# Kernel tuning notes

Measured on AMD Instinct MI355X. Metric: run time of the kernel, lower is better.

## Reference

```python
import jax, jax.numpy as jnp
import numpy as np
from jax import lax

B, E, D, N, R, K = 4, 768, 1536, 16, 48, 4
H, W = 16, 16
L = H * W
NDIR = 4


def _perms():
    idx = np.arange(L)
    idx_v = np.arange(L).reshape(H, W).T.reshape(-1)  # column-major (vertical) scan order
    perms = [idx, idx[::-1].copy(), idx_v, idx_v[::-1].copy()]
    invs = [np.argsort(p) for p in perms]
    return [jnp.asarray(p) for p in perms], [jnp.asarray(p) for p in invs]

PERMS, INVS = _perms()


def setup_inputs() -> dict:
    key = jax.random.key(0)
    ks = jax.random.split(key, 10)
    hidden_states = jax.random.normal(ks[0], (B, L, E), jnp.float32)
    in_proj_w = jax.random.normal(ks[1], (2 * D, E), jnp.float32) * 0.02
    out_proj_w = jax.random.normal(ks[2], (E, D), jnp.float32) * 0.02
    conv_w = jax.random.normal(ks[3], (NDIR, D, K), jnp.float32) * 0.1
    conv_b = jax.random.normal(ks[4], (NDIR, D), jnp.float32) * 0.1
    xproj_w = jax.random.normal(ks[5], (NDIR, R + 2 * N, D), jnp.float32) * 0.02
    dt_init_std = R ** -0.5
    dtproj_w = jax.random.uniform(ks[6], (NDIR, D, R), jnp.float32, -dt_init_std, dt_init_std)
    dt = jnp.exp(jax.random.uniform(ks[7], (NDIR, D), jnp.float32)
                 * (np.log(0.1) - np.log(0.001)) + np.log(0.001))
    dt = jnp.clip(dt, 1e-4, None)
    dtproj_b = dt + jnp.log(-jnp.expm1(-dt))  # inverse-softplus init as in the module
    A_log = jnp.broadcast_to(
        jnp.log(jnp.arange(1, N + 1, dtype=jnp.float32))[None, None, :], (NDIR, D, N)).copy()
    D_param = jnp.ones((NDIR, D), jnp.float32)
    return dict(hidden_states=hidden_states, in_proj_w=in_proj_w, out_proj_w=out_proj_w,
                conv_w=conv_w, conv_b=conv_b, xproj_w=xproj_w, dtproj_w=dtproj_w,
                dtproj_b=dtproj_b, A_log=A_log, D_param=D_param)


def _mamba_dir(xz, cw, cb, xw, dtw, dtb, a_log, dpar):
    # xz: (B, 2D, L) in this direction's scan order
    x, z = xz[:, :D], xz[:, D:]
    # causal depthwise conv1d + SiLU (mamba_inner_fn conv path)
    x = lax.conv_general_dilated(x, cw[:, None, :], (1,), [(K - 1, 0)],
                                 feature_group_count=D,
                                 dimension_numbers=('NCH', 'OIH', 'NCH'))
    x = jax.nn.silu(x + cb[None, :, None])
    # x_proj -> dt, B, C
    x_dbl = jnp.einsum('bdl,kd->bkl', x, xw)
    dt, Bm, Cm = x_dbl[:, :R], x_dbl[:, R:R + N], x_dbl[:, R + N:]
    delta = jax.nn.softplus(jnp.einsum('brl,dr->bdl', dt, dtw) + dtb[None, :, None])
    A = -jnp.exp(a_log)                                  # (D, N)
    dA = jnp.exp(jnp.einsum('bdl,dn->lbdn', delta, A))   # (L, B, D, N)
    dBu = jnp.einsum('bdl,bnl,bdl->lbdn', delta, Bm, x)  # delta * B * u

    def step(h, inp):
        da, dbu = inp
        h = da * h + dbu
        return h, h

    h0 = jnp.zeros((x.shape[0], D, N), x.dtype)
    _, hs = lax.scan(step, h0, (dA, dBu))                # (L, B, D, N)
    y = jnp.einsum('lbdn,bnl->bdl', hs, Cm) + dpar[None, :, None] * x
    return y * jax.nn.silu(z)                            # gate, (B, D, L)


def reference(hidden_states, in_proj_w, out_proj_w, conv_w, conv_b,
              xproj_w, dtproj_w, dtproj_b, A_log, D_param):
    xz = jnp.einsum('ble,fe->bfl', hidden_states, in_proj_w)  # (B, 2D, L)
    out = jnp.zeros((hidden_states.shape[0], D, L), hidden_states.dtype)
    for i in range(NDIR):  # fixed small set of structurally distinct scan directions
        xz_i = xz[:, :, PERMS[i]]
        y = _mamba_dir(xz_i, conv_w[i], conv_b[i], xproj_w[i], dtproj_w[i],
                       dtproj_b[i], A_log[i], D_param[i])
        out = out + y[:, :, INVS[i]]  # multi_reverse then sum-fusion
    return jnp.einsum('bdl,ed->ble', out, out_proj_w)
```

## Files before the change

### kernel.cpp

```cpp
#include <hip/hip_runtime.h>
#include <hip/hip_bf16.h>

#define BI   4
#define LI   256
#define EI   768
#define DI   1536
#define NI   16
#define RI   48
#define KI   4
#define NDIRS 4
#define F2D  3072
#define MROWS 1024
#define LOG2E 1.4426950408889634f

typedef float    floatx2 __attribute__((ext_vector_type(2)));
typedef float    floatx4 __attribute__((ext_vector_type(4)));
typedef _Float16 halfx2  __attribute__((ext_vector_type(2)));
typedef _Float16 halfx4  __attribute__((ext_vector_type(4)));
typedef _Float16 halfx8  __attribute__((ext_vector_type(8)));

typedef __attribute__((address_space(3))) unsigned lds_u32;
typedef __attribute__((address_space(1))) const unsigned glb_u32;

__device__ __forceinline__ void load16(const _Float16* g, _Float16* l) {
    __builtin_amdgcn_global_load_lds((glb_u32*)g, (lds_u32*)l, 16, 0, 0);
}

__device__ __forceinline__ int perm_idx(int dir, int j) {
    switch (dir) {
        case 0:  return j;
        case 1:  return 255 - j;
        case 2:  return ((j & 15) << 4) | (j >> 4);
        default: return 255 - (((j & 15) << 4) | (j >> 4));
    }
}

template<int CTRL>
__device__ __forceinline__ float dpp_add(float p) {
    int t = __builtin_amdgcn_update_dpp(0, __builtin_bit_cast(int, p),
                                        CTRL, 0xf, 0xf, true);
    return p + __builtin_bit_cast(float, t);
}
__device__ __forceinline__ float grp8_sum(float p) {
    p = dpp_add<0xB1>(p);
    p = dpp_add<0x4E>(p);
    p = dpp_add<0x141>(p);
    return p;
}

template<int BM, int BN, int WGN, int FM, int FN>
__device__ __forceinline__ void gemm_core(const _Float16* __restrict__ Ah,
                                          const _Float16* __restrict__ Al, int lda,
                                          const _Float16* __restrict__ Bh,
                                          const _Float16* __restrict__ Bl, int ldb,
                                          int nChunks, _Float16* smem,
                                          floatx4 (&acc)[FM][FN]) {
    const int tid = threadIdx.x, lane = tid & 63, wave = tid >> 6;
    const int wave_m = wave / WGN, wave_n = wave % WGN;
    _Float16* sAh = smem;
    _Float16* sAl = smem + BM * 32;
    _Float16* sBh = smem + BM * 64;
    _Float16* sBl = smem + BM * 64 + BN * 32;
    const int rr = lane & 15, koff = (lane >> 4) * 8;
    const int arow = wave_m * FM * 16, brow = wave_n * FN * 16;

    for (int c = 0; c < nChunks; ++c) {
        for (int idx = tid; idx < BM * 4; idx += 256) {
            int r = idx >> 2, s = (idx & 3) * 8;
            load16(Ah + (size_t)r * lda + c * 32 + s, sAh + idx * 8);
            load16(Al + (size_t)r * lda + c * 32 + s, sAl + idx * 8);
        }
        for (int idx = tid; idx < BN * 4; idx += 256) {
            int r = idx >> 2, s = (idx & 3) * 8;
            load16(Bh + (size_t)r * ldb + c * 32 + s, sBh + idx * 8);
            load16(Bl + (size_t)r * ldb + c * 32 + s, sBl + idx * 8);
        }
        asm volatile("s_waitcnt vmcnt(0)" ::: "memory");
        __syncthreads();

        halfx8 ahf[FM], alf[FM], bhf[FN], blf[FN];
        #pragma unroll
        for (int i = 0; i < FM; ++i) {
            ahf[i] = *(const halfx8*)(sAh + (arow + i * 16 + rr) * 32 + koff);
            alf[i] = *(const halfx8*)(sAl + (arow + i * 16 + rr) * 32 + koff);
        }
        #pragma unroll
        for (int j = 0; j < FN; ++j) {
            bhf[j] = *(const halfx8*)(sBh + (brow + j * 16 + rr) * 32 + koff);
            blf[j] = *(const halfx8*)(sBl + (brow + j * 16 + rr) * 32 + koff);
        }
        #pragma unroll
        for (int i = 0; i < FM; ++i)
            #pragma unroll
            for (int j = 0; j < FN; ++j) {
                acc[i][j] = __builtin_amdgcn_mfma_f32_16x16x32_f16(ahf[i], bhf[j], acc[i][j], 0, 0, 0);
                acc[i][j] = __builtin_amdgcn_mfma_f32_16x16x32_f16(ahf[i], blf[j], acc[i][j], 0, 0, 0);
                acc[i][j] = __builtin_amdgcn_mfma_f32_16x16x32_f16(alf[i], bhf[j], acc[i][j], 0, 0, 0);
            }
        __syncthreads();
    }
}

__global__ __launch_bounds__(256) void k_splitall(
        const float* __restrict__ hs,  const float* __restrict__ wip,
        const float* __restrict__ wop, const float* __restrict__ xw,
        const float* __restrict__ dtw,
        _Float16* __restrict__ hsh,  _Float16* __restrict__ hsl,
        _Float16* __restrict__ wiph, _Float16* __restrict__ wipl,
        _Float16* __restrict__ woph, _Float16* __restrict__ wopl,
        _Float16* __restrict__ xwh,  _Float16* __restrict__ xwl,
        _Float16* __restrict__ dtwh, _Float16* __restrict__ dtwl) {
    int i4 = (blockIdx.x * 256 + threadIdx.x) * 4;
    floatx4 v;
    _Float16 *dh, *dl; int off;
    if (i4 < 786432)        { off = i4;           v = *(const floatx4*)(hs + off);  dh = hsh;  dl = hsl;  }
    else if (i4 < 3145728)  { off = i4 - 786432;  v = *(const floatx4*)(wip + off); dh = wiph; dl = wipl; }
    else if (i4 < 4325376)  { off = i4 - 3145728; v = *(const floatx4*)(wop + off); dh = woph; dl = wopl; }
    else if (i4 < 4816896)  { off = i4 - 4325376; v = *(const floatx4*)(xw + off);  dh = xwh;  dl = xwl;  }
    else {
        int t0 = i4 - 4816896;
        int col = t0 & 63, dr = t0 >> 6;
        floatx4 z = {0.f, 0.f, 0.f, 0.f};
        v = (col < 48) ? *(const floatx4*)(dtw + (size_t)dr * 48 + col) : z;
        dh = dtwh; dl = dtwl; off = t0;
    }
    halfx4 hh, hl;
    #pragma unroll
    for (int e = 0; e < 4; ++e) {
        _Float16 h = (_Float16)v[e];
        hh[e] = h; hl[e] = (_Float16)(v[e] - (float)h);
    }
    *(halfx4*)(dh + off) = hh;
    *(halfx4*)(dl + off) = hl;
}

__global__ __launch_bounds__(256) void k_inproj_t(const _Float16* __restrict__ Ah,
                                                  const _Float16* __restrict__ Al,
                                                  const _Float16* __restrict__ Bh,
                                                  const _Float16* __restrict__ Bl,
                                                  float* __restrict__ C) {
    __shared__ _Float16 smem[128 * 64 + 128 * 64];
    int row0 = blockIdx.x * 128, col0 = blockIdx.y * 128, k0 = blockIdx.z * 384;
    float* Cp = C + (size_t)blockIdx.z * MROWS * F2D;
    floatx4 acc[4][4] = {};
    gemm_core<128, 128, 2, 4, 4>(Ah + (size_t)row0 * EI + k0, Al + (size_t)row0 * EI + k0, EI,
                                 Bh + (size_t)col0 * EI + k0, Bl + (size_t)col0 * EI + k0, EI,
                                 12, smem, acc);
    int lane = threadIdx.x & 63, wave = threadIdx.x >> 6;
    int cc = lane & 15, q = lane >> 4;
    int rbase = row0 + (wave >> 1) * 64, cbase = col0 + (wave & 1) * 64;
    #pragma unroll
    for (int i = 0; i < 4; ++i)
        #pragma unroll
        for (int j = 0; j < 4; ++j)
            #pragma unroll
            for (int r = 0; r < 4; ++r)
                Cp[(size_t)(rbase + i * 16 + q * 4 + r) * F2D + cbase + j * 16 + cc] = acc[i][j][r];
}

__global__ __launch_bounds__(256) void k_outproj_t(const _Float16* __restrict__ Ah,
                                                   const _Float16* __restrict__ Al,
                                                   const _Float16* __restrict__ Bh,
                                                   const _Float16* __restrict__ Bl,
                                                   float* __restrict__ C) {
    __shared__ _Float16 smem[192 * 64];
    int row0 = blockIdx.x * 64, col0 = blockIdx.y * 128, k0 = blockIdx.z * 384;
    float* Cp = C + (size_t)blockIdx.z * MROWS * EI;
    floatx4 acc[2][4] = {};
    gemm_core<64, 128, 2, 2, 4>(Ah + (size_t)row0 * DI + k0, Al + (size_t)row0 * DI + k0, DI,
                                Bh + (size_t)col0 * DI + k0, Bl + (size_t)col0 * DI + k0, DI,
                                12, smem, acc);
    int lane = threadIdx.x & 63, wave = threadIdx.x >> 6;
    int cc = lane & 15, q = lane >> 4;
    int rbase = row0 + (wave >> 1) * 32, cbase = col0 + (wave & 1) * 64;
    #pragma unroll
    for (int i = 0; i < 2; ++i)
        #pragma unroll
        for (int j = 0; j < 4; ++j)
            #pragma unroll
            for (int r = 0; r < 4; ++r)
                Cp[(size_t)(rbase + i * 16 + q * 4 + r) * EI + cbase + j * 16 + cc] = acc[i][j][r];
}

__global__ __launch_bounds__(256) void k_osum(const float* __restrict__ oacc,
                                              float* __restrict__ out) {
    int i4 = (blockIdx.x * 256 + threadIdx.x) * 4;
    const size_t S = (size_t)MROWS * EI;
    floatx4 s = *(const floatx4*)(oacc + i4) + *(const floatx4*)(oacc + S + i4) +
                *(const floatx4*)(oacc + 2 * S + i4) + *(const floatx4*)(oacc + 3 * S + i4);
    *(floatx4*)(out + i4) = s;
}

__global__ __launch_bounds__(256) void k_xdbl_t(const _Float16* __restrict__ xh,
                                                const _Float16* __restrict__ xl,
                                                const _Float16* __restrict__ xwh,
                                                const _Float16* __restrict__ xwl,
                                                float* __restrict__ C) {
    __shared__ _Float16 smem[208 * 64];
    int row0 = blockIdx.x * 128, dir = blockIdx.y, k0 = blockIdx.z * 192;
    float* Cp = C + (size_t)blockIdx.z * NDIRS * MROWS * 80;
    floatx4 acc[2][5] = {};
    const size_t abase = ((size_t)dir * MROWS + row0) * DI + k0;
    const size_t bbase = (size_t)dir * 80 * DI + k0;
    gemm_core<128, 80, 1, 2, 5>(xh + abase, xl + abase, DI,
                                xwh + bbase, xwl + bbase, DI, 6, smem, acc);
    int lane = threadIdx.x & 63, wave = threadIdx.x >> 6;
    int cc = lane & 15, q = lane >> 4;
    int rbase = row0 + wave * 32;
    #pragma unroll
    for (int i = 0; i < 2; ++i)
        #pragma unroll
        for (int j = 0; j < 5; ++j)
            #pragma unroll
            for (int r = 0; r < 4; ++r)
                Cp[((size_t)dir * MROWS + rbase + i * 16 + q * 4 + r) * 80 + j * 16 + cc] = acc[i][j][r];
}

__global__ __launch_bounds__(256) void k_xsplit(const float* __restrict__ acc,
                                                _Float16* __restrict__ dtqh,
                                                _Float16* __restrict__ dtql,
                                                float* __restrict__ BCm) {
    const size_t PS = (size_t)NDIRS * MROWS * 80;
    int idx = blockIdx.x * 256 + threadIdx.x;
    int dir = idx / (MROWS * 96);
    int rem = idx - dir * MROWS * 96;
    int row = rem / 96, col = rem - row * 96;
    size_t rbase = (size_t)dir * MROWS + row;
    auto sum8 = [&](int c) {
        size_t o = rbase * 80 + c;
        float s = 0.f;
        #pragma unroll
        for (int kp = 0; kp < 8; ++kp) s += acc[kp * PS + o];
        return s;
    };
    if (col < 64) {
        float v = (col < 48) ? sum8(col) : 0.f;
        _Float16 h = (_Float16)v;
        dtqh[rbase * 64 + col] = h;
        dtql[rbase * 64 + col] = (_Float16)(v - (float)h);
    } else if (col < 80) {
        int n = col - 64;
        BCm[rbase * 32 + n * 2] = sum8(48 + n);
    } else {
        int n = col - 80;
        BCm[rbase * 32 + n * 2 + 1] = sum8(64 + n);
    }
}

__global__ __launch_bounds__(256) void k_delta_t(const _Float16* __restrict__ dtqh,
                                                 const _Float16* __restrict__ dtql,
                                                 const _Float16* __restrict__ dtwh,
                                                 const _Float16* __restrict__ dtwl,
                                                 const float* __restrict__ dtb,
                                                 float* __restrict__ delta) {
    __shared__ _Float16 smem[192 * 64];
    int row0 = blockIdx.x * 64, col0 = blockIdx.y * 128, dir = blockIdx.z;
    floatx4 acc[2][4] = {};
    const size_t abase = ((size_t)dir * MROWS + row0) * 64;
    const size_t bbase = ((size_t)dir * DI + col0) * 64;
    gemm_core<64, 128, 2, 2, 4>(dtqh + abase, dtql + abase, 64,
                                dtwh + bbase, dtwl + bbase, 64, 2, smem, acc);
    int lane = threadIdx.x & 63, wave = threadIdx.x >> 6;
    int cc = lane & 15, q = lane >> 4;
    int rbase = row0 + (wave >> 1) * 32, cbase = col0 + (wave & 1) * 64;
    #pragma unroll
    for (int i = 0; i < 2; ++i)
        #pragma unroll
        for (int j = 0; j < 4; ++j) {
            int col = cbase + j * 16 + cc;
            float bias = dtb[(size_t)dir * DI + col];
            #pragma unroll
            for (int r = 0; r < 4; ++r) {
                float v = acc[i][j][r] + bias;
                float sp = (v > 20.f) ? v : log1pf(__expf(v));
                delta[((size_t)dir * MROWS + rbase + i * 16 + q * 4 + r) * DI + col] = sp;
            }
        }
}

__global__ __launch_bounds__(512) void k_conv4(const float* __restrict__ xz,
                                               const float* __restrict__ cw,
                                               const float* __restrict__ cb,
                                               _Float16* __restrict__ xh,
                                               _Float16* __restrict__ xl) {
    const size_t S = (size_t)MROWS * F2D;
    const int b = blockIdx.y, d0 = blockIdx.x * 16;
    const int tid = threadIdx.x;
    __shared__ float sx[256][18];

    for (int i = tid; i < 1024; i += 512) {
        int row = i >> 2, c4 = (i & 3) * 4;
        size_t o = ((size_t)b * 256 + row) * F2D + d0 + c4;
        floatx4 v = *(const floatx4*)(xz + o) + *(const floatx4*)(xz + S + o);
        floatx2 v0 = {v[0], v[1]}, v1 = {v[2], v[3]};
        *(floatx2*)&sx[row][c4]     = v0;
        *(floatx2*)&sx[row][c4 + 2] = v1;
    }
    __syncthreads();

    const int dsub = tid & 15, lg = tid >> 4;
    const int d = d0 + dsub, j0 = lg * 8;
    #pragma unroll
    for (int dir = 0; dir < NDIRS; ++dir) {
        floatx4 w = *(const floatx4*)(cw + ((size_t)dir * DI + d) * KI);
        float bias = cb[(size_t)dir * DI + d];
        float xm3 = (j0 >= 3) ? sx[perm_idx(dir, j0 - 3)][dsub] : 0.f;
        float xm2 = (j0 >= 2) ? sx[perm_idx(dir, j0 - 2)][dsub] : 0.f;
        float xm1 = (j0 >= 1) ? sx[perm_idx(dir, j0 - 1)][dsub] : 0.f;
        #pragma unroll
        for (int j = 0; j < 8; ++j) {
            float cur = sx[perm_idx(dir, j0 + j)][dsub];
            float s = bias + w[0] * xm3 + w[1] * xm2 + w[2] * xm1 + w[3] * cur;
            xm3 = xm2; xm2 = xm1; xm1 = cur;
            float x = s / (1.f + __expf(-s));
            _Float16 h = (_Float16)x;
            size_t o = ((size_t)dir * MROWS + b * 256 + j0 + j) * DI + d;
            xh[o] = h;
            xl[o] = (_Float16)(x - (float)h);
        }
    }
}

__global__ __launch_bounds__(256) void k_scan(const float* __restrict__ delta,
                                              const _Float16* __restrict__ xhg,
                                              const _Float16* __restrict__ xlg,
                                              const float* __restrict__ BCm,
                                              const float* __restrict__ A_log,
                                              const float* __restrict__ Dp,
                                              float* __restrict__ ydir) {
    const int dchunk = blockIdx.x, b = blockIdx.y, dir = blockIdx.z;
    const int tid = threadIdx.x;
    const int dslot = tid >> 3;
    const int np = tid & 7;
    const int d0 = dchunk * 32, d = d0 + dslot;

    __shared__ float sdx[2][32][68];
    __shared__ float sbc[2][32][32];
    __shared__ float sY[32][32];

    const float Av0 = -__expf(A_log[((size_t)dir * DI + d) * NI + 2 * np]) * LOG2E;
    const float Av1 = -__expf(A_log[((size_t)dir * DI + d) * NI + 2 * np + 1]) * LOG2E;
    const float Dpar = Dp[(size_t)dir * DI + d];
    float h0 = 0.f, h1 = 0.f;

    const size_t dirrow = (size_t)dir * MROWS;
    const int srow = tid >> 3, sc4 = (tid & 7) * 4;

    floatx4 rdel, rbc;
    halfx4 rxh, rxl;
    auto load_chunk = [&](int j0) {
        int row = b * 256 + j0 + srow;
        size_t o = (dirrow + row) * DI + d0 + sc4;
        rdel = *(const floatx4*)(delta + o);
        rxh  = *(const halfx4*)(xhg + o);
        rxl  = *(const halfx4*)(xlg + o);
        rbc  = *(const floatx4*)(BCm + (dirrow + row) * 32 + sc4);
    };

    load_chunk(0);

    for (int c = 0; c < 8; ++c) {
        const int buf = c & 1;
        #pragma unroll
        for (int e = 0; e < 4; ++e) {
            floatx2 t;
            t[0] = rdel[e];
            t[1] = (float)rxh[e] + (float)rxl[e];
            *(floatx2*)&sdx[buf][sc4 + e][srow * 2] = t;
        }
        *(floatx4*)&sbc[buf][srow][sc4] = rbc;
        __syncthreads();
        if (c < 7) load_chunk((c + 1) * 32);

        #pragma unroll
        for (int jj = 0; jj < 32; jj += 2) {
            floatx4 dxx = *(const floatx4*)&sdx[buf][dslot][jj * 2];
            #pragma unroll
            for (int t = 0; t < 2; ++t) {
                floatx4 bc = *(const floatx4*)&sbc[buf][jj + t][np * 4];
                float dv = dxx[t * 2], xv = dxx[t * 2 + 1];
                float a0 = __builtin_amdgcn_exp2f(dv * Av0);
                float a1 = __builtin_amdgcn_exp2f(dv * Av1);
                float du = dv * xv;
                h0 = fmaf(a0, h0, du * bc[0]);
                h1 = fmaf(a1, h1, du * bc[2]);
                float p = fmaf(h1, bc[3], h0 * bc[1]);
                p = grp8_sum(p);
                if (np == 0) sY[jj + t][dslot] = fmaf(Dpar, xv, p);
            }
        }
        __syncthreads();

        {
            int lout = perm_idx(dir, c * 32 + srow);
            floatx4 o = *(const floatx4*)&sY[srow][sc4];
            *(floatx4*)&ydir[(dirrow + (size_t)b * 256 + lout) * DI + d0 + sc4] = o;
        }
    }
}

__global__ __launch_bounds__(256) void k_sum(const float* __restrict__ ydir,
                                             const float* __restrict__ xz,
                                             _Float16* __restrict__ yh,
                                             _Float16* __restrict__ yl) {
    int i4 = (blockIdx.x * 256 + threadIdx.x) * 4;
    const size_t S = (size_t)MROWS * DI;
    const size_t SZ = (size_t)MROWS * F2D;
    int row = i4 / DI, dcol = i4 - row * DI;
    size_t zo = (size_t)row * F2D + DI + dcol;
    floatx4 zv = *(const floatx4*)(xz + zo) + *(const floatx4*)(xz + SZ + zo);
    floatx4 s = *(const floatx4*)(ydir + i4) + *(const floatx4*)(ydir + S + i4) +
                *(const floatx4*)(ydir + 2 * S + i4) + *(const floatx4*)(ydir + 3 * S + i4);
    halfx4 hh, hl;
    #pragma unroll
    for (int e = 0; e < 4; ++e) {
        float g = zv[e] / (1.f + __expf(-zv[e]));
        float v = s[e] * g;
        _Float16 h = (_Float16)v;
        hh[e] = h; hl[e] = (_Float16)(v - (float)h);
    }
    *(halfx4*)(yh + i4) = hh;
    *(halfx4*)(yl + i4) = hl;
}

extern "C" void kernel_launch(void* const* d_in, const int* in_sizes, int n_in,
                              void* d_out, int out_size, void* d_ws, size_t ws_size,
                              hipStream_t stream) {
    const float* hs   = (const float*)d_in[0];
    const float* wip  = (const float*)d_in[1];
    const float* wop  = (const float*)d_in[2];
    const float* cw   = (const float*)d_in[3];
    const float* cb   = (const float*)d_in[4];
    const float* xw   = (const float*)d_in[5];
    const float* dtw  = (const float*)d_in[6];
    const float* dtb  = (const float*)d_in[7];
    const float* alog = (const float*)d_in[8];
    const float* dpar = (const float*)d_in[9];
    float* out = (float*)d_out;

    char* p = (char*)d_ws;
    auto alloc_f32 = [&](size_t n) { float* r = (float*)p; p += n * 4; return r; };
    auto alloc_f16 = [&](size_t n) { _Float16* r = (_Float16*)p; p += n * 2; return r; };

    _Float16* hsh  = alloc_f16(786432);
    _Float16* hsl  = alloc_f16(786432);
    _Float16* wiph = alloc_f16(2359296);
    _Float16* wipl = alloc_f16(2359296);
    _Float16* woph = alloc_f16(1179648);
    _Float16* wopl = alloc_f16(1179648);
    _Float16* xwh  = alloc_f16(491520);
    _Float16* xwl  = alloc_f16(491520);
    _Float16* dtwh = alloc_f16((size_t)NDIRS * DI * 64);
    _Float16* dtwl = alloc_f16((size_t)NDIRS * DI * 64);
    float*    xz   = alloc_f32((size_t)2 * MROWS * F2D);
    _Float16* xh   = alloc_f16((size_t)NDIRS * MROWS * DI);
    _Float16* xl   = alloc_f16((size_t)NDIRS * MROWS * DI);
    _Float16* dtqh = alloc_f16((size_t)NDIRS * MROWS * 64);
    _Float16* dtql = alloc_f16((size_t)NDIRS * MROWS * 64);
    float*    BCm  = alloc_f32((size_t)NDIRS * MROWS * 32);
    float*    delta= alloc_f32((size_t)NDIRS * MROWS * DI);
    float*    ydir = alloc_f32((size_t)NDIRS * MROWS * DI);
    _Float16* yh   = alloc_f16((size_t)MROWS * DI);
    _Float16* yl   = alloc_f16((size_t)MROWS * DI);

    float* xdba = ydir;
    float* oacc = delta;

    k_splitall<<<dim3(5088), 256, 0, stream>>>(hs, wip, wop, xw, dtw,
                                               hsh, hsl, wiph, wipl, woph, wopl,
                                               xwh, xwl, dtwh, dtwl);
    k_inproj_t<<<dim3(8, 24, 2), 256, 0, stream>>>(hsh, hsl, wiph, wipl, xz);
    k_conv4   <<<dim3(96, BI), 512, 0, stream>>>(xz, cw, cb, xh, xl);
    k_xdbl_t  <<<dim3(8, NDIRS, 8), 256, 0, stream>>>(xh, xl, xwh, xwl, xdba);
    k_xsplit  <<<dim3(1536), 256, 0, stream>>>(xdba, dtqh, dtql, BCm);
    k_delta_t <<<dim3(16, 12, NDIRS), 256, 0, stream>>>(dtqh, dtql, dtwh, dtwl, dtb, delta);
    k_scan    <<<dim3(DI / 32, BI, NDIRS), 256, 0, stream>>>(delta, xh, xl, BCm,
                                                             alog, dpar, ydir);
    k_sum     <<<dim3(1536), 256, 0, stream>>>(ydir, xz, yh, yl);
    k_outproj_t<<<dim3(16, 6, 4), 256, 0, stream>>>(yh, yl, woph, wopl, oacc);
    k_osum    <<<dim3(768), 256, 0, stream>>>(oacc, out);
}
```

Baseline: 231.8 us.

## Fuse delta projection GEMM and softplus into the selective scan kernel

Removes the separate delta GEMM kernel. Inside the scan, each chunk of 32 timesteps now computes delta with split-fp16 MFMA (hi/lo products) from the dt-rank projections, applies the bias and softplus, and writes the result straight to shared memory. This avoids writing and re-reading the full fp32 delta tensor (4x1024x1536) through global memory and saves one launch. In exchange the scan loses its double-buffered LDS, adds a second barrier per chunk, and puts MFMA and log1p/exp work on the scan's critical path.

```diff
diff --git a/kernel.cpp b/kernel.cpp
--- a/kernel.cpp
+++ b/kernel.cpp
@@ -247,37 +247,6 @@
     }
 }
 
-__global__ __launch_bounds__(256) void k_delta_t(const _Float16* __restrict__ dtqh,
-                                                 const _Float16* __restrict__ dtql,
-                                                 const _Float16* __restrict__ dtwh,
-                                                 const _Float16* __restrict__ dtwl,
-                                                 const float* __restrict__ dtb,
-                                                 float* __restrict__ delta) {
-    __shared__ _Float16 smem[192 * 64];
-    int row0 = blockIdx.x * 64, col0 = blockIdx.y * 128, dir = blockIdx.z;
-    floatx4 acc[2][4] = {};
-    const size_t abase = ((size_t)dir * MROWS + row0) * 64;
-    const size_t bbase = ((size_t)dir * DI + col0) * 64;
-    gemm_core<64, 128, 2, 2, 4>(dtqh + abase, dtql + abase, 64,
-                                dtwh + bbase, dtwl + bbase, 64, 2, smem, acc);
-    int lane = threadIdx.x & 63, wave = threadIdx.x >> 6;
-    int cc = lane & 15, q = lane >> 4;
-    int rbase = row0 + (wave >> 1) * 32, cbase = col0 + (wave & 1) * 64;
-    #pragma unroll
-    for (int i = 0; i < 2; ++i)
-        #pragma unroll
-        for (int j = 0; j < 4; ++j) {
-            int col = cbase + j * 16 + cc;
-            float bias = dtb[(size_t)dir * DI + col];
-            #pragma unroll
-            for (int r = 0; r < 4; ++r) {
-                float v = acc[i][j][r] + bias;
-                float sp = (v > 20.f) ? v : log1pf(__expf(v));
-                delta[((size_t)dir * MROWS + rbase + i * 16 + q * 4 + r) * DI + col] = sp;
-            }
-        }
-}
-
 __global__ __launch_bounds__(512) void k_conv4(const float* __restrict__ xz,
                                                const float* __restrict__ cw,
                                                const float* __restrict__ cb,
@@ -321,7 +290,11 @@
     }
 }
 
-__global__ __launch_bounds__(256) void k_scan(const float* __restrict__ delta,
+__global__ __launch_bounds__(256) void k_scan(const _Float16* __restrict__ dtqh,
+                                              const _Float16* __restrict__ dtql,
+                                              const _Float16* __restrict__ dtwh,
+                                              const _Float16* __restrict__ dtwl,
+                                              const float* __restrict__ dtb,
                                               const _Float16* __restrict__ xhg,
                                               const _Float16* __restrict__ xlg,
                                               const float* __restrict__ BCm,
@@ -329,13 +302,13 @@
                                               const float* __restrict__ Dp,
                                               float* __restrict__ ydir) {
     const int dchunk = blockIdx.x, b = blockIdx.y, dir = blockIdx.z;
-    const int tid = threadIdx.x;
+    const int tid = threadIdx.x, lane = tid & 63, wave = tid >> 6;
     const int dslot = tid >> 3;
     const int np = tid & 7;
     const int d0 = dchunk * 32, d = d0 + dslot;
 
-    __shared__ float sdx[2][32][68];
-    __shared__ float sbc[2][32][32];
+    __shared__ float sdx[32][68];
+    __shared__ float sbc[32][32];
     __shared__ float sY[32][32];
 
     const float Av0 = -__expf(A_log[((size_t)dir * DI + d) * NI + 2 * np]) * LOG2E;
@@ -346,38 +319,68 @@
     const size_t dirrow = (size_t)dir * MROWS;
     const int srow = tid >> 3, sc4 = (tid & 7) * 4;
 
-    floatx4 rdel, rbc;
+    const int rowhalf = wave >> 1, dhalf = wave & 1;
+    const int rr = lane & 15, koff = (lane >> 4) * 8, q = lane >> 4;
+    const size_t bfb = ((size_t)dir * DI + d0 + dhalf * 16 + rr) * 64;
+    halfx8 bhf[2], blf[2];
+    bhf[0] = *(const halfx8*)(dtwh + bfb + koff);
+    bhf[1] = *(const halfx8*)(dtwh + bfb + 32 + koff);
+    blf[0] = *(const halfx8*)(dtwl + bfb + koff);
+    blf[1] = *(const halfx8*)(dtwl + bfb + 32 + koff);
+    const float bias = dtb[(size_t)dir * DI + d0 + dhalf * 16 + rr];
+
+    floatx4 rbc;
     halfx4 rxh, rxl;
     auto load_chunk = [&](int j0) {
         int row = b * 256 + j0 + srow;
         size_t o = (dirrow + row) * DI + d0 + sc4;
-        rdel = *(const floatx4*)(delta + o);
-        rxh  = *(const halfx4*)(xhg + o);
-        rxl  = *(const halfx4*)(xlg + o);
-        rbc  = *(const floatx4*)(BCm + (dirrow + row) * 32 + sc4);
+        rxh = *(const halfx4*)(xhg + o);
+        rxl = *(const halfx4*)(xlg + o);
+        rbc = *(const floatx4*)(BCm + (dirrow + row) * 32 + sc4);
     };
+    halfx8 ahf[2], alf[2];
+    auto load_afrag = [&](int c) {
+        size_t o = (dirrow + b * 256 + c * 32 + rowhalf * 16 + rr) * 64;
+        ahf[0] = *(const halfx8*)(dtqh + o + koff);
+        ahf[1] = *(const halfx8*)(dtqh + o + 32 + koff);
+        alf[0] = *(const halfx8*)(dtql + o + koff);
+        alf[1] = *(const halfx8*)(dtql + o + 32 + koff);
+    };
 
     load_chunk(0);
+    load_afrag(0);
 
     for (int c = 0; c < 8; ++c) {
-        const int buf = c & 1;
-        #pragma unroll
-        for (int e = 0; e < 4; ++e) {
-            floatx2 t;
-            t[0] = rdel[e];
-            t[1] = (float)rxh[e] + (float)rxl[e];
-            *(floatx2*)&sdx[buf][sc4 + e][srow * 2] = t;
-        }
-        *(floatx4*)&sbc[buf][srow][sc4] = rbc;
+        #pragma unroll
+        for (int e = 0; e < 4; ++e)
+            sdx[sc4 + e][srow * 2 + 1] = (float)rxh[e] + (float)rxl[e];
+        *(floatx4*)&sbc[srow][sc4] = rbc;
         __syncthreads();
-        if (c < 7) load_chunk((c + 1) * 32);
+
+        {
+            floatx4 acc = {};
+            #pragma unroll
+            for (int kc = 0; kc < 2; ++kc) {
+                acc = __builtin_amdgcn_mfma_f32_16x16x32_f16(ahf[kc], bhf[kc], acc, 0, 0, 0);
+                acc = __builtin_amdgcn_mfma_f32_16x16x32_f16(ahf[kc], blf[kc], acc, 0, 0, 0);
+                acc = __builtin_amdgcn_mfma_f32_16x16x32_f16(alf[kc], bhf[kc], acc, 0, 0, 0);
+            }
+            #pragma unroll
+            for (int r = 0; r < 4; ++r) {
+                float v = acc[r] + bias;
+                float sp = (v > 20.f) ? v : log1pf(__expf(v));
+                sdx[dhalf * 16 + rr][(rowhalf * 16 + q * 4 + r) * 2] = sp;
+            }
+        }
+        if (c < 7) { load_chunk((c + 1) * 32); load_afrag(c + 1); }
+        __syncthreads();
 
         #pragma unroll
         for (int jj = 0; jj < 32; jj += 2) {
-            floatx4 dxx = *(const floatx4*)&sdx[buf][dslot][jj * 2];
+            floatx4 dxx = *(const floatx4*)&sdx[dslot][jj * 2];
             #pragma unroll
             for (int t = 0; t < 2; ++t) {
-                floatx4 bc = *(const floatx4*)&sbc[buf][jj + t][np * 4];
+                floatx4 bc = *(const floatx4*)&sbc[jj + t][np * 4];
                 float dv = dxx[t * 2], xv = dxx[t * 2 + 1];
                 float a0 = __builtin_amdgcn_exp2f(dv * Av0);
                 float a1 = __builtin_amdgcn_exp2f(dv * Av1);
@@ -458,13 +461,12 @@
     _Float16* dtqh = alloc_f16((size_t)NDIRS * MROWS * 64);
     _Float16* dtql = alloc_f16((size_t)NDIRS * MROWS * 64);
     float*    BCm  = alloc_f32((size_t)NDIRS * MROWS * 32);
-    float*    delta= alloc_f32((size_t)NDIRS * MROWS * DI);
+    float*    oacc = alloc_f32((size_t)4 * MROWS * EI);
     float*    ydir = alloc_f32((size_t)NDIRS * MROWS * DI);
     _Float16* yh   = alloc_f16((size_t)MROWS * DI);
     _Float16* yl   = alloc_f16((size_t)MROWS * DI);
 
     float* xdba = ydir;
-    float* oacc = delta;
 
     k_splitall<<<dim3(5088), 256, 0, stream>>>(hs, wip, wop, xw, dtw,
                                                hsh, hsl, wiph, wipl, woph, wopl,
@@ -473,9 +475,8 @@
     k_conv4   <<<dim3(96, BI), 512, 0, stream>>>(xz, cw, cb, xh, xl);
     k_xdbl_t  <<<dim3(8, NDIRS, 8), 256, 0, stream>>>(xh, xl, xwh, xwl, xdba);
     k_xsplit  <<<dim3(1536), 256, 0, stream>>>(xdba, dtqh, dtql, BCm);
-    k_delta_t <<<dim3(16, 12, NDIRS), 256, 0, stream>>>(dtqh, dtql, dtwh, dtwl, dtb, delta);
-    k_scan    <<<dim3(DI / 32, BI, NDIRS), 256, 0, stream>>>(delta, xh, xl, BCm,
-                                                             alog, dpar, ydir);
+    k_scan    <<<dim3(DI / 32, BI, NDIRS), 256, 0, stream>>>(dtqh, dtql, dtwh, dtwl, dtb,
+                                                             xh, xl, BCm, alog, dpar, ydir);
     k_sum     <<<dim3(1536), 256, 0, stream>>>(ydir, xz, yh, yl);
     k_outproj_t<<<dim3(16, 6, 4), 256, 0, stream>>>(yh, yl, woph, wopl, oacc);
     k_osum    <<<dim3(768), 256, 0, stream>>>(oacc, out);
```

Measured after the change: 224.4 us. 3.2% less time.
